# Kernel optimization log

Hardware: AMD Instinct MI355X
Metric: run time of the kernel (lower is better)

Reference implementation:

```python
import jax, jax.numpy as jnp
import numpy as np


def setup_inputs() -> dict:
    key = jax.random.key(0)
    ks = jax.random.split(key, 9)
    n, L, H, H2 = 1024, 256, 512, 256
    return {
        "lstms0": jax.random.normal(ks[0], (n, L), jnp.float32),
        "lstms1": jax.random.normal(ks[1], (n, L), jnp.float32),
        "W_foh": jax.random.normal(ks[2], (2 * L, H), jnp.float32) * 0.05,
        "W_fom": jax.random.normal(ks[3], (2 * L, H), jnp.float32) * 0.05,
        "catBias": jax.random.normal(ks[4], (1, 2 * H), jnp.float32) * 0.05,
        "hid2Layer": jax.random.normal(ks[5], (2 * H, H2), jnp.float32) * 0.05,
        "hid2Bias": jax.random.normal(ks[6], (1, H2), jnp.float32) * 0.05,
        "outLayer": jax.random.normal(ks[7], (H2, 1), jnp.float32) * 0.05,
        "outBias": jax.random.normal(ks[8], (1, 1), jnp.float32) * 0.05,
    }


def reference(lstms0, lstms1, W_foh, W_fom, catBias, hid2Layer, hid2Bias, outLayer, outBias):
    act = jnp.tanh
    H = W_foh.shape[1]
    # per-token concatenated BiLSTM state: [n, 2L]
    x = jnp.concatenate([lstms0, lstms1], axis=-1)
    headfov = x @ W_foh  # [n, H]
    modfov = x @ W_fom   # [n, H]
    # activation(concat(head_i, mod_j) + catBias) is elementwise, so it splits:
    ah = act(headfov + catBias[0, :H])  # [n, H]
    am = act(modfov + catBias[0, H:])   # [n, H]
    # concat(ah_i, am_j) @ hid2Layer == ah_i @ W_top + am_j @ W_bot
    A = ah @ hid2Layer[:H]  # [n, H2]
    B = am @ hid2Layer[H:]  # [n, H2]
    # pairwise hidden: [n_head, n_mod, H2]
    Z = act(A[:, None, :] + B[None, :, :] + hid2Bias[0])
    scores = jnp.einsum("ijh,h->ij", Z, outLayer[:, 0]) + outBias[0, 0]
    return scores  # [n, n], scores[i, j] = score(head=i, mod=j)
```

## Files before the change

### kernel.cpp

```cpp
#include <hip/hip_runtime.h>
#include <hip/hip_bf16.h>

typedef short s16x4 __attribute__((ext_vector_type(4)));
typedef float f32x4 __attribute__((ext_vector_type(4)));

#define LOG2E_2 2.8853900817779268f

__device__ __forceinline__ float fexp2(float x){ return __builtin_amdgcn_exp2f(x); }
__device__ __forceinline__ float frcp (float x){ return __builtin_amdgcn_rcpf(x); }
__device__ __forceinline__ float ftanh(float v){
    return 1.0f - 2.0f * frcp(1.0f + fexp2(LOG2E_2 * v));
}
__device__ __forceinline__ unsigned short f2bf(float v){
    __hip_bfloat16 h = __float2bfloat16(v);
    return __builtin_bit_cast(unsigned short, h);
}
__device__ __forceinline__ float bf2f(unsigned short u){
    return __bfloat162float(__builtin_bit_cast(__hip_bfloat16, u));
}
__device__ __forceinline__ f32x4 mfma_bf16(s16x4 a, s16x4 b, f32x4 c){
    return __builtin_amdgcn_mfma_f32_16x16x16bf16_1k(a, b, c, 0, 0, 0);
}

__global__ __launch_bounds__(256) void prep_x(
    const float* __restrict__ l0, const float* __restrict__ l1,
    unsigned short* __restrict__ xhi, unsigned short* __restrict__ xlo)
{
    int idx = (blockIdx.x * 256 + threadIdx.x) * 4;
    int r = idx >> 9, c = idx & 511;
    float4 v = (c < 256) ? *(const float4*)(l0 + r*256 + c)
                         : *(const float4*)(l1 + r*256 + (c - 256));
    ushort4 h, l;
    h.x = f2bf(v.x); l.x = f2bf(v.x - bf2f(h.x));
    h.y = f2bf(v.y); l.y = f2bf(v.y - bf2f(h.y));
    h.z = f2bf(v.z); l.z = f2bf(v.z - bf2f(h.z));
    h.w = f2bf(v.w); l.w = f2bf(v.w - bf2f(h.w));
    *(ushort4*)(xhi + idx) = h;
    *(ushort4*)(xlo + idx) = l;
}

__global__ __launch_bounds__(256) void prep_wt(
    const float* __restrict__ srcA, const float* __restrict__ srcB,
    int splitN, int lda, int K,
    unsigned short* __restrict__ dhi, unsigned short* __restrict__ dlo)
{
    __shared__ float F[32][33];
    const int t = threadIdx.x;
    const int k0 = blockIdx.x * 32, n0 = blockIdx.y * 32;
    {
        int kk = t >> 3, n4 = (t & 7) * 4;
        int n = n0 + n4;
        const float* s = (n < splitN) ? (srcA + (k0+kk)*lda + n)
                                      : (srcB + (k0+kk)*lda + (n - splitN));
        float4 v = *(const float4*)s;
        F[kk][n4+0] = v.x; F[kk][n4+1] = v.y; F[kk][n4+2] = v.z; F[kk][n4+3] = v.w;
    }
    __syncthreads();
    {
        int nn = t >> 3, k4 = (t & 7) * 4;
        ushort4 h, l;
        float v0 = F[k4+0][nn]; h.x = f2bf(v0); l.x = f2bf(v0 - bf2f(h.x));
        float v1 = F[k4+1][nn]; h.y = f2bf(v1); l.y = f2bf(v1 - bf2f(h.y));
        float v2 = F[k4+2][nn]; h.z = f2bf(v2); l.z = f2bf(v2 - bf2f(h.z));
        float v3 = F[k4+3][nn]; h.w = f2bf(v3); l.w = f2bf(v3 - bf2f(h.w));
        *(ushort4*)(dhi + (n0+nn)*K + k0 + k4) = h;
        *(ushort4*)(dlo + (n0+nn)*K + k0 + k4) = l;
    }
}

__global__ __launch_bounds__(256) void k1_mfma(
    const unsigned short* __restrict__ xhi, const unsigned short* __restrict__ xlo,
    const unsigned short* __restrict__ whi, const unsigned short* __restrict__ wlo,
    const float* __restrict__ cb,
    unsigned short* __restrict__ hvhi, unsigned short* __restrict__ hvlo)
{
    __shared__ unsigned short Ah[64][40], Al[64][40], Bh[32][40], Bl[32][40];
    const int t = threadIdx.x;
    const int r0 = blockIdx.y * 64, c0 = blockIdx.x * 32;
    const int w = t >> 6, lane = t & 63;
    const int m = lane & 15, quad = lane >> 4;

    const int arow = t >> 2, aseg = t & 3;
    const int brow = (t & 127) >> 2, bseg = t & 3;
    const bool doB = (t < 128);

    f32x4 acc0 = {0,0,0,0}, acc1 = {0,0,0,0};

    uint4 pah = *(const uint4*)(xhi + (r0+arow)*512 + aseg*8);
    uint4 pal = *(const uint4*)(xlo + (r0+arow)*512 + aseg*8);
    uint4 pbh = {}, pbl = {};
    if (doB) {
        pbh = *(const uint4*)(whi + (c0+brow)*512 + bseg*8);
        pbl = *(const uint4*)(wlo + (c0+brow)*512 + bseg*8);
    }

    for (int c = 0; c < 16; ++c) {
        __syncthreads();
        *(uint4*)&Ah[arow][aseg*8] = pah;
        *(uint4*)&Al[arow][aseg*8] = pal;
        if (doB) {
            *(uint4*)&Bh[brow][bseg*8] = pbh;
            *(uint4*)&Bl[brow][bseg*8] = pbl;
        }
        __syncthreads();
        if (c + 1 < 16) {
            int k0 = (c+1) * 32;
            pah = *(const uint4*)(xhi + (r0+arow)*512 + k0 + aseg*8);
            pal = *(const uint4*)(xlo + (r0+arow)*512 + k0 + aseg*8);
            if (doB) {
                pbh = *(const uint4*)(whi + (c0+brow)*512 + k0 + bseg*8);
                pbl = *(const uint4*)(wlo + (c0+brow)*512 + k0 + bseg*8);
            }
        }
        #pragma unroll
        for (int ks = 0; ks < 32; ks += 16) {
            const int ko = ks + quad*4;
            s16x4 ah = *(const s16x4*)&Ah[w*16 + m][ko];
            s16x4 al = *(const s16x4*)&Al[w*16 + m][ko];
            s16x4 b0h = *(const s16x4*)&Bh[m][ko];
            s16x4 b0l = *(const s16x4*)&Bl[m][ko];
            s16x4 b1h = *(const s16x4*)&Bh[16 + m][ko];
            s16x4 b1l = *(const s16x4*)&Bl[16 + m][ko];
            acc0 = mfma_bf16(ah, b0h, acc0);
            acc0 = mfma_bf16(ah, b0l, acc0);
            acc0 = mfma_bf16(al, b0h, acc0);
            acc1 = mfma_bf16(ah, b1h, acc1);
            acc1 = mfma_bf16(ah, b1l, acc1);
            acc1 = mfma_bf16(al, b1h, acc1);
        }
    }

    #pragma unroll
    for (int nt = 0; nt < 2; ++nt) {
        f32x4 a = nt ? acc1 : acc0;
        const int col = c0 + nt*16 + m;
        const float bias = cb[col];
        #pragma unroll
        for (int reg = 0; reg < 4; ++reg) {
            const int row = r0 + w*16 + quad*4 + reg;
            float v = ftanh(a[reg] + bias);
            unsigned short h = f2bf(v);
            unsigned short l = f2bf(v - bf2f(h));
            hvhi[row*1024 + col] = h;
            hvlo[row*1024 + col] = l;
        }
    }
}

__global__ __launch_bounds__(256) void k2_mfma(
    const unsigned short* __restrict__ hvhi, const unsigned short* __restrict__ hvlo,
    const unsigned short* __restrict__ w2hi, const unsigned short* __restrict__ w2lo,
    const float* __restrict__ h2b, float* __restrict__ P)
{
    __shared__ unsigned short Ah[32][40], Al[32][40], Bh[32][40], Bl[32][40];
    const int t = threadIdx.x;
    const int r0 = blockIdx.y * 32, c0 = blockIdx.x * 32;
    const int half = (c0 >= 256) ? 1 : 0;
    const int ho = half * 512;
    const int nw = c0 & 255;
    const int w = t >> 6, lane = t & 63;
    const int m = lane & 15, quad = lane >> 4;
    const int wm = (w & 1) * 16, wn = (w >> 1) * 16;

    const int srow = (t & 127) >> 2, sseg = t & 3;
    const bool isB = (t >= 128);

    f32x4 acc = {0,0,0,0};

    uint4 ph, pl;
    if (isB) {
        ph = *(const uint4*)(w2hi + (nw+srow)*1024 + ho + sseg*8);
        pl = *(const uint4*)(w2lo + (nw+srow)*1024 + ho + sseg*8);
    } else {
        ph = *(const uint4*)(hvhi + (r0+srow)*1024 + ho + sseg*8);
        pl = *(const uint4*)(hvlo + (r0+srow)*1024 + ho + sseg*8);
    }

    for (int c = 0; c < 16; ++c) {
        __syncthreads();
        if (isB) { *(uint4*)&Bh[srow][sseg*8] = ph; *(uint4*)&Bl[srow][sseg*8] = pl; }
        else     { *(uint4*)&Ah[srow][sseg*8] = ph; *(uint4*)&Al[srow][sseg*8] = pl; }
        __syncthreads();
        if (c + 1 < 16) {
            int k0 = (c+1) * 32;
            if (isB) {
                ph = *(const uint4*)(w2hi + (nw+srow)*1024 + ho + k0 + sseg*8);
                pl = *(const uint4*)(w2lo + (nw+srow)*1024 + ho + k0 + sseg*8);
            } else {
                ph = *(const uint4*)(hvhi + (r0+srow)*1024 + ho + k0 + sseg*8);
                pl = *(const uint4*)(hvlo + (r0+srow)*1024 + ho + k0 + sseg*8);
            }
        }
        #pragma unroll
        for (int ks = 0; ks < 32; ks += 16) {
            const int ko = ks + quad*4;
            s16x4 ah = *(const s16x4*)&Ah[wm + m][ko];
            s16x4 al = *(const s16x4*)&Al[wm + m][ko];
            s16x4 bh = *(const s16x4*)&Bh[wn + m][ko];
            s16x4 bl = *(const s16x4*)&Bl[wn + m][ko];
            acc = mfma_bf16(ah, bh, acc);
            acc = mfma_bf16(ah, bl, acc);
            acc = mfma_bf16(al, bh, acc);
        }
    }

    const int col = c0 + wn + m;
    const float bias = half ? 0.0f : h2b[col];
    #pragma unroll
    for (int reg = 0; reg < 4; ++reg) {
        const int row = r0 + wm + quad*4 + reg;
        P[row*512 + col] = fexp2((acc[reg] + bias) * LOG2E_2);
    }
}

__global__ __launch_bounds__(256) void k3_pairwise(
    const float* __restrict__ P, const float* __restrict__ w,
    const float* __restrict__ ob, float* __restrict__ out)
{
    __shared__ float As[32][68];
    __shared__ float Bs[64][34];
    __shared__ float wls[256];
    const int tid = threadIdx.x;
    const int tx = tid & 15;
    const int ty = tid >> 4;
    const int i0 = blockIdx.y * 32, j0 = blockIdx.x * 32;

    wls[tid] = w[tid];

    float acc[2][2] = {};

    for (int h0 = 0; h0 < 256; h0 += 64) {
        __syncthreads();
        #pragma unroll
        for (int it = 0; it < 2; ++it) {
            int idx = tid + it*256;
            int rr  = idx >> 4;
            int c4  = (idx & 15) * 4;
            *(float4*)&As[rr][c4] = *(const float4*)&P[(i0+rr)*512 + h0 + c4];
            float4 bv = *(const float4*)&P[(j0+rr)*512 + 256 + h0 + c4];
            Bs[c4+0][rr] = bv.x;
            Bs[c4+1][rr] = bv.y;
            Bs[c4+2][rr] = bv.z;
            Bs[c4+3][rr] = bv.w;
        }
        __syncthreads();

        for (int hh = 0; hh < 64; hh += 4) {
            float4 wv = *(const float4*)&wls[h0 + hh];
            float4 a0 = *(const float4*)&As[ty*2+0][hh];
            float4 a1 = *(const float4*)&As[ty*2+1][hh];
            float2 b0 = *(const float2*)&Bs[hh+0][tx*2];
            float2 b1 = *(const float2*)&Bs[hh+1][tx*2];
            float2 b2 = *(const float2*)&Bs[hh+2][tx*2];
            float2 b3 = *(const float2*)&Bs[hh+3][tx*2];
            float aa[2][4] = {{a0.x,a0.y,a0.z,a0.w},{a1.x,a1.y,a1.z,a1.w}};
            float bb[4][2] = {{b0.x,b0.y},{b1.x,b1.y},{b2.x,b2.y},{b3.x,b3.y}};
            float ww[4] = {wv.x, wv.y, wv.z, wv.w};
            #pragma unroll
            for (int h = 0; h < 4; ++h)
                #pragma unroll
                for (int r = 0; r < 2; ++r)
                    #pragma unroll
                    for (int q = 0; q < 2; ++q) {
                        float u = fmaf(aa[r][h], bb[h][q], 1.0f);
                        acc[r][q] = fmaf(ww[h], frcp(u), acc[r][q]);
                    }
        }
    }

    float sumw = 0.0f;
    #pragma unroll
    for (int h = 0; h < 256; h += 4) {
        float4 wv = *(const float4*)&wls[h];
        sumw += (wv.x + wv.y) + (wv.z + wv.w);
    }
    const float base = ob[0] + sumw;
    const int row = i0 + ty*2;
    const int col = j0 + tx*2;
    #pragma unroll
    for (int r = 0; r < 2; ++r) {
        float2 o;
        o.x = base - 2.0f*acc[r][0];
        o.y = base - 2.0f*acc[r][1];
        *(float2*)&out[(row+r)*1024 + col] = o;
    }
}

extern "C" void kernel_launch(void* const* d_in, const int* in_sizes, int n_in,
                              void* d_out, int out_size, void* d_ws, size_t ws_size,
                              hipStream_t stream) {
    const float* l0   = (const float*)d_in[0];
    const float* l1   = (const float*)d_in[1];
    const float* Wfoh = (const float*)d_in[2];
    const float* Wfom = (const float*)d_in[3];
    const float* cb   = (const float*)d_in[4];
    const float* W2   = (const float*)d_in[5];
    const float* h2b  = (const float*)d_in[6];
    const float* w    = (const float*)d_in[7];
    const float* ob   = (const float*)d_in[8];
    float* out = (float*)d_out;

    unsigned short* hv_hi  = (unsigned short*)d_ws;
    unsigned short* hv_lo  = hv_hi + 1024*1024;
    float*          P      = (float*)(hv_lo + 1024*1024);
    unsigned short* xs_hi  = (unsigned short*)(P + 1024*512);
    unsigned short* xs_lo  = xs_hi + 1024*512;
    unsigned short* w1t_hi = xs_lo + 1024*512;
    unsigned short* w1t_lo = w1t_hi + 1024*512;
    unsigned short* w2t_hi = w1t_lo + 1024*512;
    unsigned short* w2t_lo = w2t_hi + 256*1024;

    prep_x<<<512, 256, 0, stream>>>(l0, l1, xs_hi, xs_lo);
    prep_wt<<<dim3(16,32), 256, 0, stream>>>(Wfoh, Wfom, 512, 512, 512, w1t_hi, w1t_lo);
    prep_wt<<<dim3(32,8),  256, 0, stream>>>(W2, W2, 1<<30, 256, 1024, w2t_hi, w2t_lo);
    k1_mfma<<<dim3(32,16), 256, 0, stream>>>(xs_hi, xs_lo, w1t_hi, w1t_lo, cb, hv_hi, hv_lo);
    k2_mfma<<<dim3(16,32), 256, 0, stream>>>(hv_hi, hv_lo, w2t_hi, w2t_lo, h2b, P);
    k3_pairwise<<<dim3(32,32), 256, 0, stream>>>(P, w, ob, out);
}
```

Baseline: 135.2 us.

## Use 16x16x32 bf16 MFMA, enlarge k2 tiles, prefetch k3 pairwise loads

Switches the split-bf16 GEMMs in k1 and k2 to the 16x16x32 bf16 MFMA, so each 32-wide K chunk needs one instruction per product instead of two. k2 is retiled to 64x32 blocks with two accumulators per wave, like k1, which halves the grid and increases B-tile reuse. k3 now register-prefetches the next P chunk while the current one is computed, to overlap global loads with the reciprocal-heavy inner loop. The bigger k2 tile cuts the block count, which may reduce occupancy, and k3 holds extra registers.

```diff
diff --git a/kernel.cpp b/kernel.cpp
--- a/kernel.cpp
+++ b/kernel.cpp
@@ -2,6 +2,7 @@
 #include <hip/hip_bf16.h>
 
 typedef short s16x4 __attribute__((ext_vector_type(4)));
+typedef short s16x8 __attribute__((ext_vector_type(8)));
 typedef float f32x4 __attribute__((ext_vector_type(4)));
 
 #define LOG2E_2 2.8853900817779268f
@@ -18,8 +19,8 @@
 __device__ __forceinline__ float bf2f(unsigned short u){
     return __bfloat162float(__builtin_bit_cast(__hip_bfloat16, u));
 }
-__device__ __forceinline__ f32x4 mfma_bf16(s16x4 a, s16x4 b, f32x4 c){
-    return __builtin_amdgcn_mfma_f32_16x16x16bf16_1k(a, b, c, 0, 0, 0);
+__device__ __forceinline__ f32x4 mfma32(s16x8 a, s16x8 b, f32x4 c){
+    return __builtin_amdgcn_mfma_f32_16x16x32_bf16(a, b, c, 0, 0, 0);
 }
 
 __global__ __launch_bounds__(256) void prep_x(
@@ -86,13 +87,15 @@
 
     f32x4 acc0 = {0,0,0,0}, acc1 = {0,0,0,0};
 
-    uint4 pah = *(const uint4*)(xhi + (r0+arow)*512 + aseg*8);
-    uint4 pal = *(const uint4*)(xlo + (r0+arow)*512 + aseg*8);
+    const unsigned short* pAh = xhi + (r0+arow)*512 + aseg*8;
+    const unsigned short* pAl = xlo + (r0+arow)*512 + aseg*8;
+    const unsigned short* pBh = whi + (c0+brow)*512 + bseg*8;
+    const unsigned short* pBl = wlo + (c0+brow)*512 + bseg*8;
+
+    uint4 pah = *(const uint4*)pAh;
+    uint4 pal = *(const uint4*)pAl;
     uint4 pbh = {}, pbl = {};
-    if (doB) {
-        pbh = *(const uint4*)(whi + (c0+brow)*512 + bseg*8);
-        pbl = *(const uint4*)(wlo + (c0+brow)*512 + bseg*8);
-    }
+    if (doB) { pbh = *(const uint4*)pBh; pbl = *(const uint4*)pBl; }
 
     for (int c = 0; c < 16; ++c) {
         __syncthreads();
@@ -105,28 +108,27 @@
         __syncthreads();
         if (c + 1 < 16) {
             int k0 = (c+1) * 32;
-            pah = *(const uint4*)(xhi + (r0+arow)*512 + k0 + aseg*8);
-            pal = *(const uint4*)(xlo + (r0+arow)*512 + k0 + aseg*8);
+            pah = *(const uint4*)(pAh + k0);
+            pal = *(const uint4*)(pAl + k0);
             if (doB) {
-                pbh = *(const uint4*)(whi + (c0+brow)*512 + k0 + bseg*8);
-                pbl = *(const uint4*)(wlo + (c0+brow)*512 + k0 + bseg*8);
+                pbh = *(const uint4*)(pBh + k0);
+                pbl = *(const uint4*)(pBl + k0);
             }
         }
-        #pragma unroll
-        for (int ks = 0; ks < 32; ks += 16) {
-            const int ko = ks + quad*4;
-            s16x4 ah = *(const s16x4*)&Ah[w*16 + m][ko];
-            s16x4 al = *(const s16x4*)&Al[w*16 + m][ko];
-            s16x4 b0h = *(const s16x4*)&Bh[m][ko];
-            s16x4 b0l = *(const s16x4*)&Bl[m][ko];
-            s16x4 b1h = *(const s16x4*)&Bh[16 + m][ko];
-            s16x4 b1l = *(const s16x4*)&Bl[16 + m][ko];
-            acc0 = mfma_bf16(ah, b0h, acc0);
-            acc0 = mfma_bf16(ah, b0l, acc0);
-            acc0 = mfma_bf16(al, b0h, acc0);
-            acc1 = mfma_bf16(ah, b1h, acc1);
-            acc1 = mfma_bf16(ah, b1l, acc1);
-            acc1 = mfma_bf16(al, b1h, acc1);
+        {
+            const int ko = quad*8;
+            s16x8 ah  = *(const s16x8*)&Ah[w*16 + m][ko];
+            s16x8 al  = *(const s16x8*)&Al[w*16 + m][ko];
+            s16x8 b0h = *(const s16x8*)&Bh[m][ko];
+            s16x8 b0l = *(const s16x8*)&Bl[m][ko];
+            s16x8 b1h = *(const s16x8*)&Bh[16 + m][ko];
+            s16x8 b1l = *(const s16x8*)&Bl[16 + m][ko];
+            acc0 = mfma32(ah, b0h, acc0);
+            acc0 = mfma32(ah, b0l, acc0);
+            acc0 = mfma32(al, b0h, acc0);
+            acc1 = mfma32(ah, b1h, acc1);
+            acc1 = mfma32(ah, b1l, acc1);
+            acc1 = mfma32(al, b1h, acc1);
         }
     }
 
@@ -152,64 +154,76 @@
     const unsigned short* __restrict__ w2hi, const unsigned short* __restrict__ w2lo,
     const float* __restrict__ h2b, float* __restrict__ P)
 {
-    __shared__ unsigned short Ah[32][40], Al[32][40], Bh[32][40], Bl[32][40];
+    __shared__ unsigned short Ah[64][40], Al[64][40], Bh[32][40], Bl[32][40];
     const int t = threadIdx.x;
-    const int r0 = blockIdx.y * 32, c0 = blockIdx.x * 32;
+    const int r0 = blockIdx.y * 64, c0 = blockIdx.x * 32;
     const int half = (c0 >= 256) ? 1 : 0;
     const int ho = half * 512;
     const int nw = c0 & 255;
     const int w = t >> 6, lane = t & 63;
     const int m = lane & 15, quad = lane >> 4;
-    const int wm = (w & 1) * 16, wn = (w >> 1) * 16;
-
-    const int srow = (t & 127) >> 2, sseg = t & 3;
-    const bool isB = (t >= 128);
-
-    f32x4 acc = {0,0,0,0};
-
-    uint4 ph, pl;
-    if (isB) {
-        ph = *(const uint4*)(w2hi + (nw+srow)*1024 + ho + sseg*8);
-        pl = *(const uint4*)(w2lo + (nw+srow)*1024 + ho + sseg*8);
-    } else {
-        ph = *(const uint4*)(hvhi + (r0+srow)*1024 + ho + sseg*8);
-        pl = *(const uint4*)(hvlo + (r0+srow)*1024 + ho + sseg*8);
-    }
+
+    const int arow = t >> 2, aseg = t & 3;
+    const int brow = (t & 127) >> 2, bseg = t & 3;
+    const bool doB = (t < 128);
+
+    f32x4 acc0 = {0,0,0,0}, acc1 = {0,0,0,0};
+
+    const unsigned short* pAh = hvhi + (r0+arow)*1024 + ho + aseg*8;
+    const unsigned short* pAl = hvlo + (r0+arow)*1024 + ho + aseg*8;
+    const unsigned short* pBh = w2hi + (nw+brow)*1024 + ho + bseg*8;
+    const unsigned short* pBl = w2lo + (nw+brow)*1024 + ho + bseg*8;
+
+    uint4 pah = *(const uint4*)pAh;
+    uint4 pal = *(const uint4*)pAl;
+    uint4 pbh = {}, pbl = {};
+    if (doB) { pbh = *(const uint4*)pBh; pbl = *(const uint4*)pBl; }
 
     for (int c = 0; c < 16; ++c) {
         __syncthreads();
-        if (isB) { *(uint4*)&Bh[srow][sseg*8] = ph; *(uint4*)&Bl[srow][sseg*8] = pl; }
-        else     { *(uint4*)&Ah[srow][sseg*8] = ph; *(uint4*)&Al[srow][sseg*8] = pl; }
+        *(uint4*)&Ah[arow][aseg*8] = pah;
+        *(uint4*)&Al[arow][aseg*8] = pal;
+        if (doB) {
+            *(uint4*)&Bh[brow][bseg*8] = pbh;
+            *(uint4*)&Bl[brow][bseg*8] = pbl;
+        }
         __syncthreads();
         if (c + 1 < 16) {
             int k0 = (c+1) * 32;
-            if (isB) {
-                ph = *(const uint4*)(w2hi + (nw+srow)*1024 + ho + k0 + sseg*8);
-                pl = *(const uint4*)(w2lo + (nw+srow)*1024 + ho + k0 + sseg*8);
-            } else {
-                ph = *(const uint4*)(hvhi + (r0+srow)*1024 + ho + k0 + sseg*8);
-                pl = *(const uint4*)(hvlo + (r0+srow)*1024 + ho + k0 + sseg*8);
+            pah = *(const uint4*)(pAh + k0);
+            pal = *(const uint4*)(pAl + k0);
+            if (doB) {
+                pbh = *(const uint4*)(pBh + k0);
+                pbl = *(const uint4*)(pBl + k0);
             }
         }
+        {
+            const int ko = quad*8;
+            s16x8 ah  = *(const s16x8*)&Ah[w*16 + m][ko];
+            s16x8 al  = *(const s16x8*)&Al[w*16 + m][ko];
+            s16x8 b0h = *(const s16x8*)&Bh[m][ko];
+            s16x8 b0l = *(const s16x8*)&Bl[m][ko];
+            s16x8 b1h = *(const s16x8*)&Bh[16 + m][ko];
+            s16x8 b1l = *(const s16x8*)&Bl[16 + m][ko];
+            acc0 = mfma32(ah, b0h, acc0);
+            acc0 = mfma32(ah, b0l, acc0);
+            acc0 = mfma32(al, b0h, acc0);
+            acc1 = mfma32(ah, b1h, acc1);
+            acc1 = mfma32(ah, b1l, acc1);
+            acc1 = mfma32(al, b1h, acc1);
+        }
+    }
+
+    #pragma unroll
+    for (int nt = 0; nt < 2; ++nt) {
+        f32x4 a = nt ? acc1 : acc0;
+        const int col = c0 + nt*16 + m;
+        const float bias = half ? 0.0f : h2b[col];
         #pragma unroll
-        for (int ks = 0; ks < 32; ks += 16) {
-            const int ko = ks + quad*4;
-            s16x4 ah = *(const s16x4*)&Ah[wm + m][ko];
-            s16x4 al = *(const s16x4*)&Al[wm + m][ko];
-            s16x4 bh = *(const s16x4*)&Bh[wn + m][ko];
-            s16x4 bl = *(const s16x4*)&Bl[wn + m][ko];
-            acc = mfma_bf16(ah, bh, acc);
-            acc = mfma_bf16(ah, bl, acc);
-            acc = mfma_bf16(al, bh, acc);
-        }
-    }
-
-    const int col = c0 + wn + m;
-    const float bias = half ? 0.0f : h2b[col];
-    #pragma unroll
-    for (int reg = 0; reg < 4; ++reg) {
-        const int row = r0 + wm + quad*4 + reg;
-        P[row*512 + col] = fexp2((acc[reg] + bias) * LOG2E_2);
+        for (int reg = 0; reg < 4; ++reg) {
+            const int row = r0 + w*16 + quad*4 + reg;
+            P[row*512 + col] = fexp2((a[reg] + bias) * LOG2E_2);
+        }
     }
 }
 
@@ -227,26 +241,35 @@
 
     wls[tid] = w[tid];
 
+    int rr0 = tid >> 4,        c40 = (tid & 15) * 4;
+    int rr1 = (tid + 256) >> 4, c41 = (tid & 15) * 4;
+
     float acc[2][2] = {};
 
-    for (int h0 = 0; h0 < 256; h0 += 64) {
-        __syncthreads();
-        #pragma unroll
-        for (int it = 0; it < 2; ++it) {
-            int idx = tid + it*256;
-            int rr  = idx >> 4;
-            int c4  = (idx & 15) * 4;
-            *(float4*)&As[rr][c4] = *(const float4*)&P[(i0+rr)*512 + h0 + c4];
-            float4 bv = *(const float4*)&P[(j0+rr)*512 + 256 + h0 + c4];
-            Bs[c4+0][rr] = bv.x;
-            Bs[c4+1][rr] = bv.y;
-            Bs[c4+2][rr] = bv.z;
-            Bs[c4+3][rr] = bv.w;
-        }
-        __syncthreads();
+    float4 pa0 = *(const float4*)&P[(i0+rr0)*512 + 0 + c40];
+    float4 pa1 = *(const float4*)&P[(i0+rr1)*512 + 0 + c41];
+    float4 pb0 = *(const float4*)&P[(j0+rr0)*512 + 256 + 0 + c40];
+    float4 pb1 = *(const float4*)&P[(j0+rr1)*512 + 256 + 0 + c41];
+
+    for (int c = 0; c < 4; ++c) {
+        __syncthreads();
+        *(float4*)&As[rr0][c40] = pa0;
+        *(float4*)&As[rr1][c41] = pa1;
+        Bs[c40+0][rr0] = pb0.x; Bs[c40+1][rr0] = pb0.y;
+        Bs[c40+2][rr0] = pb0.z; Bs[c40+3][rr0] = pb0.w;
+        Bs[c41+0][rr1] = pb1.x; Bs[c41+1][rr1] = pb1.y;
+        Bs[c41+2][rr1] = pb1.z; Bs[c41+3][rr1] = pb1.w;
+        __syncthreads();
+        if (c + 1 < 4) {
+            int h0 = (c+1) * 64;
+            pa0 = *(const float4*)&P[(i0+rr0)*512 + h0 + c40];
+            pa1 = *(const float4*)&P[(i0+rr1)*512 + h0 + c41];
+            pb0 = *(const float4*)&P[(j0+rr0)*512 + 256 + h0 + c40];
+            pb1 = *(const float4*)&P[(j0+rr1)*512 + 256 + h0 + c41];
+        }
 
         for (int hh = 0; hh < 64; hh += 4) {
-            float4 wv = *(const float4*)&wls[h0 + hh];
+            float4 wv = *(const float4*)&wls[c*64 + hh];
             float4 a0 = *(const float4*)&As[ty*2+0][hh];
             float4 a1 = *(const float4*)&As[ty*2+1][hh];
             float2 b0 = *(const float2*)&Bs[hh+0][tx*2];
@@ -314,6 +337,6 @@
     prep_wt<<<dim3(16,32), 256, 0, stream>>>(Wfoh, Wfom, 512, 512, 512, w1t_hi, w1t_lo);
     prep_wt<<<dim3(32,8),  256, 0, stream>>>(W2, W2, 1<<30, 256, 1024, w2t_hi, w2t_lo);
     k1_mfma<<<dim3(32,16), 256, 0, stream>>>(xs_hi, xs_lo, w1t_hi, w1t_lo, cb, hv_hi, hv_lo);
-    k2_mfma<<<dim3(16,32), 256, 0, stream>>>(hv_hi, hv_lo, w2t_hi, w2t_lo, h2b, P);
+    k2_mfma<<<dim3(16,16), 256, 0, stream>>>(hv_hi, hv_lo, w2t_hi, w2t_lo, h2b, P);
     k3_pairwise<<<dim3(32,32), 256, 0, stream>>>(P, w, ob, out);
 }
```

Result: faster. 131.0 us (-3.1%).
